# Performance work log

Measured on AMD Instinct MI355X. Metric: run time of the kernel, lower is better.

Reference implementation:

```python
import jax, jax.numpy as jnp
import numpy as np

M, H, D, P = 16, 32, 128, 8192
N = H * D


def setup_inputs() -> dict:
    key = jax.random.key(0)
    k1, k2, k3, k4, k5, k6 = jax.random.split(key, 6)
    X = jax.random.normal(k1, (M, N), dtype=jnp.float32)
    # small init scale keeps the module's naive (unstabilized) exp-softmax finite
    Wq = jax.random.normal(k2, (N, N), dtype=jnp.float32) * 0.02
    Wk = jax.random.normal(k3, (N, N), dtype=jnp.float32) * 0.02
    Wv = jax.random.normal(k4, (N, N), dtype=jnp.float32) * 0.02
    cache_K = jax.random.normal(k5, (H, P, D), dtype=jnp.float32) * 0.05
    cache_V = jax.random.normal(k6, (H, P, D), dtype=jnp.float32)
    return {"X": X, "Wq": Wq, "Wk": Wk, "Wv": Wv,
            "cache_K": cache_K, "cache_V": cache_V}


def reference(X, Wq, Wk, Wv, cache_K, cache_V):
    m, n = X.shape                      # [M, N]
    h, p, d = cache_K.shape             # [H, P, D]
    # RMSNorm (no learned scale, matches (X*X).sum / N)
    x2 = jnp.sum(X * X, axis=1)
    x_norm = X / jnp.sqrt(x2 / n)[:, None]
    # QKV projections (nn.Linear, no bias -> x @ W.T)
    q = (x_norm @ Wq.T).reshape(m, h, d).transpose(1, 0, 2)   # [H, M, D]
    k = (x_norm @ Wk.T).reshape(m, h, d).transpose(1, 0, 2)   # [H, M, D]
    v = (x_norm @ Wv.T).reshape(m, h, d).transpose(1, 0, 2)   # [H, M, D]
    # append to cache
    ck = jnp.concatenate([cache_K, k], axis=1)                # [H, P+M, D]
    cv = jnp.concatenate([cache_V, v], axis=1)                # [H, P+M, D]
    # scores (no 1/sqrt(D) scaling in the original) + naive softmax
    c = jnp.einsum('hmd,hpd->hmp', q, ck)                     # [H, M, P+M]
    c_exp = jnp.exp(c)
    c_div = c_exp / jnp.sum(c_exp, axis=2, keepdims=True)
    o = jnp.einsum('hmp,hpd->hmd', c_div, cv)                 # [H, M, D]
    return o.transpose(1, 0, 2).reshape(m, n)                 # [M, N]
```

## Files before the change

kernel.cpp:

```cpp
#include <hip/hip_runtime.h>

#define NN 4096
#define HH 32
#define DD 128
#define MM 16
#define PP 8192

__device__ __forceinline__ float4 ld4(const float* p) { return *(const float4*)(p); }
__device__ __forceinline__ float dot4f(float4 a, float4 b) {
  return a.x * b.x + a.y * b.y + a.z * b.z + a.w * b.w;
}

__global__ void k1_rms(const float* __restrict__ X, float* __restrict__ inv) {
  const int m = blockIdx.x;
  const int tid = threadIdx.x;
  float s = 0.f;
#pragma unroll
  for (int i = 0; i < 16; ++i) {
    float v = X[(size_t)m * NN + i * 256 + tid];
    s += v * v;
  }
#pragma unroll
  for (int off = 1; off < 64; off <<= 1) s += __shfl_xor(s, off, 64);
  __shared__ float red[4];
  if ((tid & 63) == 0) red[tid >> 6] = s;
  __syncthreads();
  if (tid == 0) {
    float t = red[0] + red[1] + red[2] + red[3];
    inv[m] = rsqrtf(t * (1.0f / (float)NN));
  }
}

__global__ __launch_bounds__(256, 3) void k2_qkv(
    const float* __restrict__ X, const float* __restrict__ Wq,
    const float* __restrict__ Wk, const float* __restrict__ Wv,
    float* __restrict__ c_part) {
  __shared__ float wt[2][4][1024];
  __shared__ float lds_c[4][32][17];
  const int b = blockIdx.x;
  const int mat = b >> 9;
  const int qt = (b >> 7) & 3;
  const int rb = b & 127;
  const float* W = (mat == 0) ? Wq : (mat == 1) ? Wk : Wv;
  const int tid = threadIdx.x;
  const int wave = tid >> 6;
  const int lane = tid & 63;
  const int m4 = lane & 3;
  const int g = lane >> 2;
  const int kwin = wave * 256 + g * 16;
  const int kbase = qt * 1024 + kwin;

  float4 xr[4][4];
#pragma unroll
  for (int mi = 0; mi < 4; ++mi) {
    const float* xp = X + (size_t)(mi * 4 + m4) * NN + kbase;
#pragma unroll
    for (int j = 0; j < 4; ++j) xr[mi][j] = ld4(xp + j * 4);
  }

  const float* Wbase = W + (size_t)(rb * 32) * NN + qt * 1024;
  float4 rw[4];
#pragma unroll
  for (int i = 0; i < 4; ++i) {
    const int id = tid + i * 256;
    rw[i] = *((const float4*)(Wbase + (size_t)(id >> 8) * NN) + (id & 255));
  }

  for (int tt = 0; tt < 8; ++tt) {
    __syncthreads();
#pragma unroll
    for (int i = 0; i < 4; ++i)
      ((float4*)wt[tt & 1])[tid + i * 256] = rw[i];
    __syncthreads();
    if (tt < 7) {
      const float* Wn = Wbase + (size_t)((tt + 1) * 4) * NN;
#pragma unroll
      for (int i = 0; i < 4; ++i) {
        const int id = tid + i * 256;
        rw[i] = *((const float4*)(Wn + (size_t)(id >> 8) * NN) + (id & 255));
      }
    }
    float acc[4][4];
#pragma unroll
    for (int r = 0; r < 4; ++r)
#pragma unroll
      for (int mi = 0; mi < 4; ++mi) acc[r][mi] = 0.f;
#pragma unroll
    for (int r = 0; r < 4; ++r) {
      const float* wp = wt[tt & 1][r] + kwin;
      float4 w0 = ld4(wp), w1 = ld4(wp + 4), w2 = ld4(wp + 8), w3 = ld4(wp + 12);
#pragma unroll
      for (int mi = 0; mi < 4; ++mi)
        acc[r][mi] += dot4f(xr[mi][0], w0) + dot4f(xr[mi][1], w1) +
                      dot4f(xr[mi][2], w2) + dot4f(xr[mi][3], w3);
    }
#pragma unroll
    for (int off = 4; off < 64; off <<= 1)
#pragma unroll
      for (int r = 0; r < 4; ++r)
#pragma unroll
        for (int mi = 0; mi < 4; ++mi)
          acc[r][mi] += __shfl_xor(acc[r][mi], off, 64);
    if (g == 0) {
#pragma unroll
      for (int r = 0; r < 4; ++r)
#pragma unroll
        for (int mi = 0; mi < 4; ++mi)
          lds_c[wave][tt * 4 + r][mi * 4 + m4] = acc[r][mi];
    }
  }
  __syncthreads();
#pragma unroll
  for (int i = 0; i < 2; ++i) {
    const int idx = i * 256 + tid;
    const int l = idx >> 4;
    const int m = idx & 15;
    float s = lds_c[0][l][m] + lds_c[1][l][m] + lds_c[2][l][m] + lds_c[3][l][m];
    c_part[(((size_t)(mat * 4 + qt) * 16 + m) << 12) + (rb * 32 + l)] = s;
  }
}

__global__ void k2b_combine(const float* __restrict__ c_part,
                            const float* __restrict__ inv,
                            float* __restrict__ qkv) {
  const int t = blockIdx.x * 256 + threadIdx.x;
  const int mat = t >> 16;
  const int r = t & 65535;
  const int m = r >> 12;
  const int j = r & 4095;
  float s = 0.f;
#pragma unroll
  for (int qt = 0; qt < 4; ++qt)
    s += c_part[(((size_t)(mat * 4 + qt) * 16 + m) << 12) + j];
  qkv[(((size_t)(mat * 16 + m)) << 12) + j] = s * inv[m];
}

__global__ __launch_bounds__(256, 2) void k3_attn(
    const float* __restrict__ cK, const float* __restrict__ cV,
    const float* __restrict__ qkv, float* __restrict__ o_part,
    float* __restrict__ den_part) {
  __shared__ float sK[2][4096];
  __shared__ float sV[2][4096];
  const int b = blockIdx.x;
  const int h = b >> 4;
  const int seg = b & 15;
  const int tid = threadIdx.x;
  const int wave = tid >> 6;
  const int lane = tid & 63;
  const int m8 = lane & 7;
  const int g = lane >> 3;
  const int d0 = g * 16;

  float4 q0[4], q1[4];
  {
    const float* qa = qkv + (size_t)m8 * NN + h * DD + d0;
    const float* qb = qkv + (size_t)(m8 + 8) * NN + h * DD + d0;
#pragma unroll
    for (int j = 0; j < 4; ++j) { q0[j] = ld4(qa + j * 4); q1[j] = ld4(qb + j * 4); }
  }
  float o0[16], o1[16];
#pragma unroll
  for (int j = 0; j < 16; ++j) { o0[j] = 0.f; o1[j] = 0.f; }
  float den0 = 0.f, den1 = 0.f;

  const float4* gK = (const float4*)(cK + ((size_t)h * PP + seg * 512) * DD);
  const float4* gV = (const float4*)(cV + ((size_t)h * PP + seg * 512) * DD);

  float4 rk[4], rv[4];
#pragma unroll
  for (int i = 0; i < 4; ++i) { rk[i] = gK[tid + i * 256]; rv[i] = gV[tid + i * 256]; }

  for (int t = 0; t < 16; ++t) {
    __syncthreads();
#pragma unroll
    for (int i = 0; i < 4; ++i) {
      ((float4*)sK[t & 1])[tid + i * 256] = rk[i];
      ((float4*)sV[t & 1])[tid + i * 256] = rv[i];
    }
    __syncthreads();
    if (t < 15) {
      const int base = (t + 1) * 1024;
#pragma unroll
      for (int i = 0; i < 4; ++i) {
        rk[i] = gK[base + tid + i * 256];
        rv[i] = gV[base + tid + i * 256];
      }
    }
    const float* bK = sK[t & 1];
    const float* bV = sV[t & 1];
#pragma unroll
    for (int pi = 0; pi < 8; ++pi) {
      const int p = wave * 8 + pi;
      const float* kp = bK + p * DD + d0;
      float4 k0 = ld4(kp), k1 = ld4(kp + 4), k2 = ld4(kp + 8), k3 = ld4(kp + 12);
      float c0 = dot4f(q0[0], k0) + dot4f(q0[1], k1) + dot4f(q0[2], k2) + dot4f(q0[3], k3);
      float c1 = dot4f(q1[0], k0) + dot4f(q1[1], k1) + dot4f(q1[2], k2) + dot4f(q1[3], k3);
#pragma unroll
      for (int off = 8; off < 64; off <<= 1) {
        c0 += __shfl_xor(c0, off, 64);
        c1 += __shfl_xor(c1, off, 64);
      }
      float e0 = __expf(c0), e1 = __expf(c1);
      den0 += e0; den1 += e1;
      const float* vp = bV + p * DD + d0;
      float4 v0 = ld4(vp), v1 = ld4(vp + 4), v2 = ld4(vp + 8), v3 = ld4(vp + 12);
      o0[0] += e0 * v0.x;  o0[1] += e0 * v0.y;  o0[2] += e0 * v0.z;  o0[3] += e0 * v0.w;
      o0[4] += e0 * v1.x;  o0[5] += e0 * v1.y;  o0[6] += e0 * v1.z;  o0[7] += e0 * v1.w;
      o0[8] += e0 * v2.x;  o0[9] += e0 * v2.y;  o0[10] += e0 * v2.z; o0[11] += e0 * v2.w;
      o0[12] += e0 * v3.x; o0[13] += e0 * v3.y; o0[14] += e0 * v3.z; o0[15] += e0 * v3.w;
      o1[0] += e1 * v0.x;  o1[1] += e1 * v0.y;  o1[2] += e1 * v0.z;  o1[3] += e1 * v0.w;
      o1[4] += e1 * v1.x;  o1[5] += e1 * v1.y;  o1[6] += e1 * v1.z;  o1[7] += e1 * v1.w;
      o1[8] += e1 * v2.x;  o1[9] += e1 * v2.y;  o1[10] += e1 * v2.z; o1[11] += e1 * v2.w;
      o1[12] += e1 * v3.x; o1[13] += e1 * v3.y; o1[14] += e1 * v3.z; o1[15] += e1 * v3.w;
    }
  }

  if (seg == (h & 15)) {
    __syncthreads();
    const int r0 = tid >> 5;
    const int c = tid & 31;
#pragma unroll
    for (int rr = 0; rr < 2; ++rr) {
      const int p = rr * 8 + r0;
      ((float4*)sK[0])[p * 32 + c] =
          *((const float4*)(qkv + (size_t)(16 + p) * NN + h * DD) + c);
      ((float4*)sV[0])[p * 32 + c] =
          *((const float4*)(qkv + (size_t)(32 + p) * NN + h * DD) + c);
    }
    __syncthreads();
#pragma unroll
    for (int pi = 0; pi < 4; ++pi) {
      const int p = wave * 4 + pi;
      const float* kp = sK[0] + p * DD + d0;
      float4 k0 = ld4(kp), k1 = ld4(kp + 4), k2 = ld4(kp + 8), k3 = ld4(kp + 12);
      float c0 = dot4f(q0[0], k0) + dot4f(q0[1], k1) + dot4f(q0[2], k2) + dot4f(q0[3], k3);
      float c1 = dot4f(q1[0], k0) + dot4f(q1[1], k1) + dot4f(q1[2], k2) + dot4f(q1[3], k3);
#pragma unroll
      for (int off = 8; off < 64; off <<= 1) {
        c0 += __shfl_xor(c0, off, 64);
        c1 += __shfl_xor(c1, off, 64);
      }
      float e0 = __expf(c0), e1 = __expf(c1);
      den0 += e0; den1 += e1;
      const float* vp = sV[0] + p * DD + d0;
      float4 v0 = ld4(vp), v1 = ld4(vp + 4), v2 = ld4(vp + 8), v3 = ld4(vp + 12);
      o0[0] += e0 * v0.x;  o0[1] += e0 * v0.y;  o0[2] += e0 * v0.z;  o0[3] += e0 * v0.w;
      o0[4] += e0 * v1.x;  o0[5] += e0 * v1.y;  o0[6] += e0 * v1.z;  o0[7] += e0 * v1.w;
      o0[8] += e0 * v2.x;  o0[9] += e0 * v2.y;  o0[10] += e0 * v2.z; o0[11] += e0 * v2.w;
      o0[12] += e0 * v3.x; o0[13] += e0 * v3.y; o0[14] += e0 * v3.z; o0[15] += e0 * v3.w;
      o1[0] += e1 * v0.x;  o1[1] += e1 * v0.y;  o1[2] += e1 * v0.z;  o1[3] += e1 * v0.w;
      o1[4] += e1 * v1.x;  o1[5] += e1 * v1.y;  o1[6] += e1 * v1.z;  o1[7] += e1 * v1.w;
      o1[8] += e1 * v2.x;  o1[9] += e1 * v2.y;  o1[10] += e1 * v2.z; o1[11] += e1 * v2.w;
      o1[12] += e1 * v3.x; o1[13] += e1 * v3.y; o1[14] += e1 * v3.z; o1[15] += e1 * v3.w;
    }
  }

  float* op = o_part + ((size_t)b * 4 + wave) * 2048;
#pragma unroll
  for (int j = 0; j < 4; ++j) {
    *(float4*)(op + m8 * DD + d0 + j * 4) =
        make_float4(o0[j * 4], o0[j * 4 + 1], o0[j * 4 + 2], o0[j * 4 + 3]);
    *(float4*)(op + (m8 + 8) * DD + d0 + j * 4) =
        make_float4(o1[j * 4], o1[j * 4 + 1], o1[j * 4 + 2], o1[j * 4 + 3]);
  }
  if (g == 0) {
    den_part[((size_t)b * 4 + wave) * 16 + m8] = den0;
    den_part[((size_t)b * 4 + wave) * 16 + 8 + m8] = den1;
  }
}

__global__ void k4_final(const float* __restrict__ o_part,
                         const float* __restrict__ den_part,
                         float* __restrict__ out) {
  const int b = blockIdx.x;
  const int h = b >> 3;
  const int tid = threadIdx.x;
  const int idx = (b & 7) * 256 + tid;
  __shared__ float dinv[16];
  if (tid < 16) {
    float s = 0.f;
    for (int j = 0; j < 64; ++j) s += den_part[(size_t)h * 1024 + j * 16 + tid];
    dinv[tid] = 1.0f / s;
  }
  __syncthreads();
  float s = 0.f;
  for (int j = 0; j < 64; ++j) s += o_part[(size_t)h * 131072 + j * 2048 + idx];
  const int m = idx >> 7;
  const int d = idx & 127;
  out[(size_t)m * NN + h * DD + d] = s * dinv[m];
}

extern "C" void kernel_launch(void* const* d_in, const int* in_sizes, int n_in,
                              void* d_out, int out_size, void* d_ws, size_t ws_size,
                              hipStream_t stream) {
  (void)in_sizes; (void)n_in; (void)out_size; (void)ws_size;
  const float* X  = (const float*)d_in[0];
  const float* Wq = (const float*)d_in[1];
  const float* Wk = (const float*)d_in[2];
  const float* Wv = (const float*)d_in[3];
  const float* cK = (const float*)d_in[4];
  const float* cV = (const float*)d_in[5];
  float* out = (float*)d_out;
  float* ws = (float*)d_ws;

  float* inv      = ws;
  float* c_part   = ws + 16;
  float* qkv      = c_part + 786432;
  float* o_part   = qkv + 196608;
  float* den_part = o_part + 4194304;

  k1_rms<<<16, 256, 0, stream>>>(X, inv);
  k2_qkv<<<1536, 256, 0, stream>>>(X, Wq, Wk, Wv, c_part);
  k2b_combine<<<768, 256, 0, stream>>>(c_part, inv, qkv);
  k3_attn<<<dim3(512), 256, 0, stream>>>(cK, cV, qkv, o_part, den_part);
  k4_final<<<256, 256, 0, stream>>>(o_part, den_part, out);
}
```

Baseline: 478.8 us.

## Drop LDS staging in QKV GEMV and attention, stream directly to registers

The QKV projection kernel is retiled so each wave loads its own W rows straight into double-buffered registers, split-K 16 ways. It reduces with a butterfly shuffle that transposes partial sums across lanes, removing the LDS staging and __syncthreads. The combine kernel now sums 16 partials in a new c_part layout, which needs a larger workspace. The attention kernel likewise drops shared-memory K/V tiles: each wave streams its own 128 cache rows into registers with two-deep prefetch, removing barriers and LDS traffic. The risk is uncoalesced per-lane float4 loads, less latency hiding, and extra partial-sum traffic in the combine step.

```diff
diff --git a/kernel.cpp b/kernel.cpp
--- a/kernel.cpp
+++ b/kernel.cpp
@@ -35,88 +35,87 @@
     const float* __restrict__ X, const float* __restrict__ Wq,
     const float* __restrict__ Wk, const float* __restrict__ Wv,
     float* __restrict__ c_part) {
-  __shared__ float wt[2][4][1024];
-  __shared__ float lds_c[4][32][17];
   const int b = blockIdx.x;
-  const int mat = b >> 9;
-  const int qt = (b >> 7) & 3;
-  const int rb = b & 127;
+  const int mat = b >> 8;
+  const int rem = b & 255;
+  const int kw = rem >> 4;
+  const int rblk = rem & 15;
   const float* W = (mat == 0) ? Wq : (mat == 1) ? Wk : Wv;
   const int tid = threadIdx.x;
   const int wave = tid >> 6;
   const int lane = tid & 63;
   const int m4 = lane & 3;
   const int g = lane >> 2;
-  const int kwin = wave * 256 + g * 16;
-  const int kbase = qt * 1024 + kwin;
+  const int r0 = rblk * 256 + wave * 64;
+  const int koff = kw * 256 + g * 16;
 
   float4 xr[4][4];
 #pragma unroll
   for (int mi = 0; mi < 4; ++mi) {
-    const float* xp = X + (size_t)(mi * 4 + m4) * NN + kbase;
+    const float* xp = X + (size_t)(mi * 4 + m4) * NN + koff;
 #pragma unroll
     for (int j = 0; j < 4; ++j) xr[mi][j] = ld4(xp + j * 4);
   }
 
-  const float* Wbase = W + (size_t)(rb * 32) * NN + qt * 1024;
-  float4 rw[4];
-#pragma unroll
-  for (int i = 0; i < 4; ++i) {
-    const int id = tid + i * 256;
-    rw[i] = *((const float4*)(Wbase + (size_t)(id >> 8) * NN) + (id & 255));
-  }
-
-  for (int tt = 0; tt < 8; ++tt) {
-    __syncthreads();
-#pragma unroll
-    for (int i = 0; i < 4; ++i)
-      ((float4*)wt[tt & 1])[tid + i * 256] = rw[i];
-    __syncthreads();
-    if (tt < 7) {
-      const float* Wn = Wbase + (size_t)((tt + 1) * 4) * NN;
+  const float* Wb = W + (size_t)r0 * NN + koff;
+  const size_t cb = ((size_t)(mat * 16 + kw)) * 65536;
+
+  float4 wb[2][2][4];
+#pragma unroll
+  for (int r = 0; r < 2; ++r) {
+    const float* wr = Wb + (size_t)r * NN;
+#pragma unroll
+    for (int j = 0; j < 4; ++j) wb[0][r][j] = ld4(wr + j * 4);
+  }
+
+  for (int bt = 0; bt < 32; ++bt) {
+    const int ph = bt & 1;
+    if (bt < 31) {
+#pragma unroll
+      for (int r = 0; r < 2; ++r) {
+        const float* wr = Wb + (size_t)((bt + 1) * 2 + r) * NN;
+#pragma unroll
+        for (int j = 0; j < 4; ++j) wb[ph ^ 1][r][j] = ld4(wr + j * 4);
+      }
+    }
+    float v[8];
+#pragma unroll
+    for (int i = 0; i < 8; ++i) v[i] = 0.f;
+#pragma unroll
+    for (int r = 0; r < 2; ++r)
+#pragma unroll
+      for (int j = 0; j < 4; ++j)
+#pragma unroll
+        for (int mi = 0; mi < 4; ++mi)
+          v[r * 4 + mi] += dot4f(xr[mi][j], wb[ph][r][j]);
+    {
+      const bool u32 = (lane & 32) != 0;
 #pragma unroll
       for (int i = 0; i < 4; ++i) {
-        const int id = tid + i * 256;
-        rw[i] = *((const float4*)(Wn + (size_t)(id >> 8) * NN) + (id & 255));
-      }
-    }
-    float acc[4][4];
-#pragma unroll
-    for (int r = 0; r < 4; ++r)
-#pragma unroll
-      for (int mi = 0; mi < 4; ++mi) acc[r][mi] = 0.f;
-#pragma unroll
-    for (int r = 0; r < 4; ++r) {
-      const float* wp = wt[tt & 1][r] + kwin;
-      float4 w0 = ld4(wp), w1 = ld4(wp + 4), w2 = ld4(wp + 8), w3 = ld4(wp + 12);
-#pragma unroll
-      for (int mi = 0; mi < 4; ++mi)
-        acc[r][mi] += dot4f(xr[mi][0], w0) + dot4f(xr[mi][1], w1) +
-                      dot4f(xr[mi][2], w2) + dot4f(xr[mi][3], w3);
-    }
-#pragma unroll
-    for (int off = 4; off < 64; off <<= 1)
-#pragma unroll
-      for (int r = 0; r < 4; ++r)
-#pragma unroll
-        for (int mi = 0; mi < 4; ++mi)
-          acc[r][mi] += __shfl_xor(acc[r][mi], off, 64);
-    if (g == 0) {
-#pragma unroll
-      for (int r = 0; r < 4; ++r)
-#pragma unroll
-        for (int mi = 0; mi < 4; ++mi)
-          lds_c[wave][tt * 4 + r][mi * 4 + m4] = acc[r][mi];
-    }
-  }
-  __syncthreads();
-#pragma unroll
-  for (int i = 0; i < 2; ++i) {
-    const int idx = i * 256 + tid;
-    const int l = idx >> 4;
-    const int m = idx & 15;
-    float s = lds_c[0][l][m] + lds_c[1][l][m] + lds_c[2][l][m] + lds_c[3][l][m];
-    c_part[(((size_t)(mat * 4 + qt) * 16 + m) << 12) + (rb * 32 + l)] = s;
+        float send = u32 ? v[i] : v[i + 4];
+        float recv = __shfl_xor(send, 32, 64);
+        v[i] = (u32 ? v[i + 4] : v[i]) + recv;
+      }
+      const bool u16 = (lane & 16) != 0;
+#pragma unroll
+      for (int i = 0; i < 2; ++i) {
+        float send = u16 ? v[i] : v[i + 2];
+        float recv = __shfl_xor(send, 16, 64);
+        v[i] = (u16 ? v[i + 2] : v[i]) + recv;
+      }
+      const bool u8 = (lane & 8) != 0;
+      {
+        float send = u8 ? v[0] : v[1];
+        float recv = __shfl_xor(send, 8, 64);
+        v[0] = (u8 ? v[1] : v[0]) + recv;
+      }
+      v[0] += __shfl_xor(v[0], 4, 64);
+    }
+    if (!(lane & 4)) {
+      const int row = r0 + bt * 2 + (g >> 3);
+      const int m = ((g >> 1) & 3) * 4 + m4;
+      c_part[cb + (size_t)row * 16 + m] = v[0];
+    }
   }
 }
 
@@ -130,8 +129,8 @@
   const int j = r & 4095;
   float s = 0.f;
 #pragma unroll
-  for (int qt = 0; qt < 4; ++qt)
-    s += c_part[(((size_t)(mat * 4 + qt) * 16 + m) << 12) + j];
+  for (int kw = 0; kw < 16; ++kw)
+    s += c_part[((size_t)(mat * 16 + kw)) * 65536 + (size_t)j * 16 + m];
   qkv[(((size_t)(mat * 16 + m)) << 12) + j] = s * inv[m];
 }
 
@@ -139,8 +138,6 @@
     const float* __restrict__ cK, const float* __restrict__ cV,
     const float* __restrict__ qkv, float* __restrict__ o_part,
     float* __restrict__ den_part) {
-  __shared__ float sK[2][4096];
-  __shared__ float sV[2][4096];
   const int b = blockIdx.x;
   const int h = b >> 4;
   const int seg = b & 15;
@@ -163,97 +160,71 @@
   for (int j = 0; j < 16; ++j) { o0[j] = 0.f; o1[j] = 0.f; }
   float den0 = 0.f, den1 = 0.f;
 
-  const float4* gK = (const float4*)(cK + ((size_t)h * PP + seg * 512) * DD);
-  const float4* gV = (const float4*)(cV + ((size_t)h * PP + seg * 512) * DD);
-
-  float4 rk[4], rv[4];
-#pragma unroll
-  for (int i = 0; i < 4; ++i) { rk[i] = gK[tid + i * 256]; rv[i] = gV[tid + i * 256]; }
-
-  for (int t = 0; t < 16; ++t) {
-    __syncthreads();
-#pragma unroll
-    for (int i = 0; i < 4; ++i) {
-      ((float4*)sK[t & 1])[tid + i * 256] = rk[i];
-      ((float4*)sV[t & 1])[tid + i * 256] = rv[i];
-    }
-    __syncthreads();
-    if (t < 15) {
-      const int base = (t + 1) * 1024;
-#pragma unroll
-      for (int i = 0; i < 4; ++i) {
-        rk[i] = gK[base + tid + i * 256];
-        rv[i] = gV[base + tid + i * 256];
-      }
-    }
-    const float* bK = sK[t & 1];
-    const float* bV = sV[t & 1];
-#pragma unroll
-    for (int pi = 0; pi < 8; ++pi) {
-      const int p = wave * 8 + pi;
-      const float* kp = bK + p * DD + d0;
-      float4 k0 = ld4(kp), k1 = ld4(kp + 4), k2 = ld4(kp + 8), k3 = ld4(kp + 12);
-      float c0 = dot4f(q0[0], k0) + dot4f(q0[1], k1) + dot4f(q0[2], k2) + dot4f(q0[3], k3);
-      float c1 = dot4f(q1[0], k0) + dot4f(q1[1], k1) + dot4f(q1[2], k2) + dot4f(q1[3], k3);
-#pragma unroll
-      for (int off = 8; off < 64; off <<= 1) {
-        c0 += __shfl_xor(c0, off, 64);
-        c1 += __shfl_xor(c1, off, 64);
-      }
-      float e0 = __expf(c0), e1 = __expf(c1);
-      den0 += e0; den1 += e1;
-      const float* vp = bV + p * DD + d0;
-      float4 v0 = ld4(vp), v1 = ld4(vp + 4), v2 = ld4(vp + 8), v3 = ld4(vp + 12);
-      o0[0] += e0 * v0.x;  o0[1] += e0 * v0.y;  o0[2] += e0 * v0.z;  o0[3] += e0 * v0.w;
-      o0[4] += e0 * v1.x;  o0[5] += e0 * v1.y;  o0[6] += e0 * v1.z;  o0[7] += e0 * v1.w;
-      o0[8] += e0 * v2.x;  o0[9] += e0 * v2.y;  o0[10] += e0 * v2.z; o0[11] += e0 * v2.w;
-      o0[12] += e0 * v3.x; o0[13] += e0 * v3.y; o0[14] += e0 * v3.z; o0[15] += e0 * v3.w;
-      o1[0] += e1 * v0.x;  o1[1] += e1 * v0.y;  o1[2] += e1 * v0.z;  o1[3] += e1 * v0.w;
-      o1[4] += e1 * v1.x;  o1[5] += e1 * v1.y;  o1[6] += e1 * v1.z;  o1[7] += e1 * v1.w;
-      o1[8] += e1 * v2.x;  o1[9] += e1 * v2.y;  o1[10] += e1 * v2.z; o1[11] += e1 * v2.w;
-      o1[12] += e1 * v3.x; o1[13] += e1 * v3.y; o1[14] += e1 * v3.z; o1[15] += e1 * v3.w;
-    }
+  const size_t rowb = ((size_t)h * PP + seg * 512 + wave * 128) * DD;
+  const float* kb = cK + rowb + d0;
+  const float* vb = cV + rowb + d0;
+
+  float4 kA[4], vA[4], kB[4], vB[4];
+#pragma unroll
+  for (int j = 0; j < 4; ++j) { kA[j] = ld4(kb + j * 4); vA[j] = ld4(vb + j * 4); }
+
+#define K3_COMPUTE(KR, VR)                                                     \
+  {                                                                            \
+    float c0 = dot4f(q0[0], KR[0]) + dot4f(q0[1], KR[1]) +                     \
+               dot4f(q0[2], KR[2]) + dot4f(q0[3], KR[3]);                      \
+    float c1 = dot4f(q1[0], KR[0]) + dot4f(q1[1], KR[1]) +                     \
+               dot4f(q1[2], KR[2]) + dot4f(q1[3], KR[3]);                      \
+    c0 += __shfl_xor(c0, 8, 64);  c1 += __shfl_xor(c1, 8, 64);                 \
+    c0 += __shfl_xor(c0, 16, 64); c1 += __shfl_xor(c1, 16, 64);                \
+    c0 += __shfl_xor(c0, 32, 64); c1 += __shfl_xor(c1, 32, 64);                \
+    float e0 = __expf(c0), e1 = __expf(c1);                                    \
+    den0 += e0; den1 += e1;                                                    \
+    o0[0] += e0 * VR[0].x;  o0[1] += e0 * VR[0].y;                             \
+    o0[2] += e0 * VR[0].z;  o0[3] += e0 * VR[0].w;                             \
+    o0[4] += e0 * VR[1].x;  o0[5] += e0 * VR[1].y;                             \
+    o0[6] += e0 * VR[1].z;  o0[7] += e0 * VR[1].w;                             \
+    o0[8] += e0 * VR[2].x;  o0[9] += e0 * VR[2].y;                             \
+    o0[10] += e0 * VR[2].z; o0[11] += e0 * VR[2].w;                            \
+    o0[12] += e0 * VR[3].x; o0[13] += e0 * VR[3].y;                            \
+    o0[14] += e0 * VR[3].z; o0[15] += e0 * VR[3].w;                            \
+    o1[0] += e1 * VR[0].x;  o1[1] += e1 * VR[0].y;                             \
+    o1[2] += e1 * VR[0].z;  o1[3] += e1 * VR[0].w;                             \
+    o1[4] += e1 * VR[1].x;  o1[5] += e1 * VR[1].y;                             \
+    o1[6] += e1 * VR[1].z;  o1[7] += e1 * VR[1].w;                             \
+    o1[8] += e1 * VR[2].x;  o1[9] += e1 * VR[2].y;                             \
+    o1[10] += e1 * VR[2].z; o1[11] += e1 * VR[2].w;                            \
+    o1[12] += e1 * VR[3].x; o1[13] += e1 * VR[3].y;                            \
+    o1[14] += e1 * VR[3].z; o1[15] += e1 * VR[3].w;                            \
+  }
+
+  for (int pi = 0; pi < 128; pi += 2) {
+    const float* kn = kb + (size_t)(pi + 1) * DD;
+    const float* vn = vb + (size_t)(pi + 1) * DD;
+#pragma unroll
+    for (int j = 0; j < 4; ++j) { kB[j] = ld4(kn + j * 4); vB[j] = ld4(vn + j * 4); }
+    K3_COMPUTE(kA, vA)
+    if (pi + 2 < 128) {
+      const float* kn2 = kb + (size_t)(pi + 2) * DD;
+      const float* vn2 = vb + (size_t)(pi + 2) * DD;
+#pragma unroll
+      for (int j = 0; j < 4; ++j) { kA[j] = ld4(kn2 + j * 4); vA[j] = ld4(vn2 + j * 4); }
+    }
+    K3_COMPUTE(kB, vB)
   }
 
   if (seg == (h & 15)) {
-    __syncthreads();
-    const int r0 = tid >> 5;
-    const int c = tid & 31;
-#pragma unroll
-    for (int rr = 0; rr < 2; ++rr) {
-      const int p = rr * 8 + r0;
-      ((float4*)sK[0])[p * 32 + c] =
-          *((const float4*)(qkv + (size_t)(16 + p) * NN + h * DD) + c);
-      ((float4*)sV[0])[p * 32 + c] =
-          *((const float4*)(qkv + (size_t)(32 + p) * NN + h * DD) + c);
-    }
-    __syncthreads();
 #pragma unroll
     for (int pi = 0; pi < 4; ++pi) {
       const int p = wave * 4 + pi;
-      const float* kp = sK[0] + p * DD + d0;
-      float4 k0 = ld4(kp), k1 = ld4(kp + 4), k2 = ld4(kp + 8), k3 = ld4(kp + 12);
-      float c0 = dot4f(q0[0], k0) + dot4f(q0[1], k1) + dot4f(q0[2], k2) + dot4f(q0[3], k3);
-      float c1 = dot4f(q1[0], k0) + dot4f(q1[1], k1) + dot4f(q1[2], k2) + dot4f(q1[3], k3);
-#pragma unroll
-      for (int off = 8; off < 64; off <<= 1) {
-        c0 += __shfl_xor(c0, off, 64);
-        c1 += __shfl_xor(c1, off, 64);
-      }
-      float e0 = __expf(c0), e1 = __expf(c1);
-      den0 += e0; den1 += e1;
-      const float* vp = sV[0] + p * DD + d0;
-      float4 v0 = ld4(vp), v1 = ld4(vp + 4), v2 = ld4(vp + 8), v3 = ld4(vp + 12);
-      o0[0] += e0 * v0.x;  o0[1] += e0 * v0.y;  o0[2] += e0 * v0.z;  o0[3] += e0 * v0.w;
-      o0[4] += e0 * v1.x;  o0[5] += e0 * v1.y;  o0[6] += e0 * v1.z;  o0[7] += e0 * v1.w;
-      o0[8] += e0 * v2.x;  o0[9] += e0 * v2.y;  o0[10] += e0 * v2.z; o0[11] += e0 * v2.w;
-      o0[12] += e0 * v3.x; o0[13] += e0 * v3.y; o0[14] += e0 * v3.z; o0[15] += e0 * v3.w;
-      o1[0] += e1 * v0.x;  o1[1] += e1 * v0.y;  o1[2] += e1 * v0.z;  o1[3] += e1 * v0.w;
-      o1[4] += e1 * v1.x;  o1[5] += e1 * v1.y;  o1[6] += e1 * v1.z;  o1[7] += e1 * v1.w;
-      o1[8] += e1 * v2.x;  o1[9] += e1 * v2.y;  o1[10] += e1 * v2.z; o1[11] += e1 * v2.w;
-      o1[12] += e1 * v3.x; o1[13] += e1 * v3.y; o1[14] += e1 * v3.z; o1[15] += e1 * v3.w;
-    }
-  }
+      const float* kp = qkv + (size_t)(16 + p) * NN + h * DD + d0;
+      const float* vp = qkv + (size_t)(32 + p) * NN + h * DD + d0;
+      float4 kr[4], vr[4];
+#pragma unroll
+      for (int j = 0; j < 4; ++j) { kr[j] = ld4(kp + j * 4); vr[j] = ld4(vp + j * 4); }
+      K3_COMPUTE(kr, vr)
+    }
+  }
+#undef K3_COMPUTE
 
   float* op = o_part + ((size_t)b * 4 + wave) * 2048;
 #pragma unroll
@@ -305,13 +276,13 @@
 
   float* inv      = ws;
   float* c_part   = ws + 16;
-  float* qkv      = c_part + 786432;
+  float* qkv      = c_part + 3145728;
   float* o_part   = qkv + 196608;
   float* den_part = o_part + 4194304;
 
   k1_rms<<<16, 256, 0, stream>>>(X, inv);
-  k2_qkv<<<1536, 256, 0, stream>>>(X, Wq, Wk, Wv, c_part);
+  k2_qkv<<<768, 256, 0, stream>>>(X, Wq, Wk, Wv, c_part);
   k2b_combine<<<768, 256, 0, stream>>>(c_part, inv, qkv);
-  k3_attn<<<dim3(512), 256, 0, stream>>>(cK, cV, qkv, o_part, den_part);
+  k3_attn<<<512, 256, 0, stream>>>(cK, cV, qkv, o_part, den_part);
   k4_final<<<256, 256, 0, stream>>>(o_part, den_part, out);
 }
```

Measured after the change: 767.3 us. +60.3%, slower.
